# Kernel optimization log

Measured on AMD Instinct MI355X. Metric: run time of the kernel, lower is better.

Reference implementation:

```python
import jax, jax.numpy as jnp
import numpy as np

B, D, N, K = 16, 128, 4096, 1024


def setup_inputs() -> dict:
    key = jax.random.key(0)
    k1, k2 = jax.random.split(key)
    ze = jax.random.normal(k1, (B, D, N), dtype=jnp.float32)
    emb = jax.random.normal(k2, (K, D), dtype=jnp.float32)
    return {"ze": ze, "emb": emb}


def reference(ze, emb):
    """VQ forward: nearest-codebook quantization with straight-through estimator.

    ze:  (B, D, N) encoder latents (D = n_latent_dim, N = timesteps)
    emb: (K, D) codebook (stop-gradient applied, matching StopGrad on emb)
    returns zq_rg: (B, D, N) quantized latents; gradient flows straight to ze
    (ReplaceGrad: zq gets zero grad, ze gets the output grad).
    """
    emb_sg = jax.lax.stop_gradient(emb)
    # Squared L2 distance via expansion, avoiding the (B, D, K, N) broadcast:
    # d2[b,k,n] = ||ze[b,:,n]||^2 + ||emb[k]||^2 - 2 <ze[b,:,n], emb[k]>
    ze_sq = jnp.sum(ze * ze, axis=1)            # (B, N)
    emb_sq = jnp.sum(emb_sg * emb_sg, axis=1)   # (K,)
    dot = jnp.einsum('bdn,kd->bkn', ze, emb_sg)  # (B, K, N)
    d2 = ze_sq[:, None, :] + emb_sq[None, :, None] - 2.0 * dot
    ind = jnp.argmin(d2, axis=1)                # (B, N) nearest codebook index
    zq = jnp.transpose(jnp.take(emb_sg, ind, axis=0), (0, 2, 1))  # (B, D, N)
    # ReplaceGrad straight-through: value of zq, gradient routed to ze.
    zq_rg = ze + jax.lax.stop_gradient(zq - ze)
    return zq_rg
```

## Files before the change

kernel.cpp:

```cpp
#include <hip/hip_runtime.h>
#include <hip/hip_bf16.h>
#include <math.h>

#define BB 16
#define DD 128
#define NN 4096
#define KK 1024
#define CADD 320.0f
#define TAU 0.45f

typedef __attribute__((ext_vector_type(8))) short short8;
typedef __attribute__((ext_vector_type(4))) float f32x4;

static __device__ __forceinline__ unsigned short f32_bf16_rne(float f) {
    unsigned u = __float_as_uint(f);
    u += 0x7FFF + ((u >> 16) & 1);
    return (unsigned short)(u >> 16);
}
static __device__ __forceinline__ unsigned umin32(unsigned a, unsigned b) { return a < b ? a : b; }
static __device__ __forceinline__ unsigned umax32(unsigned a, unsigned b) { return a > b ? a : b; }
static __device__ __forceinline__ unsigned umed3(unsigned a, unsigned b, unsigned c) {
    unsigned d;
    asm("v_med3_u32 %0, %1, %2, %3" : "=v"(d) : "v"(a), "v"(b), "v"(c));
    return d;
}

__global__ void emb_sq_kernel(const float* __restrict__ emb,
                              float* __restrict__ e2) {
    int k = blockIdx.x * 256 + threadIdx.x;
    if (k >= KK) return;
    const float4* row = reinterpret_cast<const float4*>(emb + (size_t)k * DD);
    float a0 = 0.f, a1 = 0.f, a2 = 0.f, a3 = 0.f;
#pragma unroll
    for (int i = 0; i < DD / 16; ++i) {
        float4 v0 = row[i * 4 + 0];
        float4 v1 = row[i * 4 + 1];
        float4 v2 = row[i * 4 + 2];
        float4 v3 = row[i * 4 + 3];
        a0 += v0.x * v0.x + v0.y * v0.y + v0.z * v0.z + v0.w * v0.w;
        a1 += v1.x * v1.x + v1.y * v1.y + v1.z * v1.z + v1.w * v1.w;
        a2 += v2.x * v2.x + v2.y * v2.y + v2.z * v2.z + v2.w * v2.w;
        a3 += v3.x * v3.x + v3.y * v3.y + v3.z * v3.z + v3.w * v3.w;
    }
    e2[k] = (a0 + a1) + (a2 + a3) + CADD;
}

__global__ void emb_pack_kernel(const float* __restrict__ emb,
                                short* __restrict__ epk) {
    int g = blockIdx.x * 256 + threadIdx.x;
    int lane = g & 63;
    int s    = (g >> 6) & 3;
    int t    = g >> 8;
    int k = t * 16 + (lane & 15);
    int d = s * 32 + ((lane >> 4) & 3) * 8;
    const float* src = emb + (size_t)k * DD + d;
    short8 h;
#pragma unroll
    for (int j = 0; j < 8; ++j) h[j] = (short)f32_bf16_rne(-2.0f * src[j]);
    *reinterpret_cast<short8*>(epk + (size_t)g * 8) = h;
}

#define CEU(a, b) { unsigned lo_ = umin32(a, b), hi_ = umax32(a, b); (a) = lo_; (b) = hi_; }
#define MRG9(A1, A2, A3, A4, B1, B2, B3, B4) \
    CEU(A1, B1) CEU(A2, B2) CEU(A3, B3) CEU(A4, B4) \
    CEU(A3, B1) CEU(A4, B2) \
    CEU(A2, A3) \
    CEU(A4, B1) \
    CEU(A3, A4)

__global__ __launch_bounds__(256, 4)
void vq_mfma(const float* __restrict__ ze, const float* __restrict__ emb,
             const short* __restrict__ epk, const float* __restrict__ e2,
             float* __restrict__ out) {
    __shared__ __align__(16) char ubuf[(DD + 1) * 32 * 4];
    __shared__ unsigned kbuf[4][32][4];
    __shared__ int winner_s[32];
    __shared__ int rlist[32];
    __shared__ int rcnt;

    short* zstage = reinterpret_cast<short*>(ubuf);

    const int tid  = threadIdx.x;
    const int lane = tid & 63;
    const int wave = tid >> 6;
    const int b    = blockIdx.x >> 7;
    const int n0b  = (blockIdx.x & 127) * 32;
    const float* zb = ze + (size_t)b * DD * NN;

    const int nq = lane & 15;
    const int dq = (lane >> 4) & 3;

    float* e2w = reinterpret_cast<float*>(ubuf + 8192) + wave * 256;

#pragma unroll
    for (int cg = 0; cg < 2; ++cg) {
        const int col = n0b + cg * 16 + nq;
        const int d0  = wave * 32 + dq * 8;
        const float* zp = zb + (size_t)d0 * NN + col;
        short8 h;
#pragma unroll
        for (int j = 0; j < 8; ++j) h[j] = (short)f32_bf16_rne(zp[(size_t)j * NN]);
        *reinterpret_cast<short8*>(zstage + (cg * 256 + wave * 64 + lane) * 8) = h;
    }
#pragma unroll
    for (int i = 0; i < 4; ++i)
        e2w[i * 64 + lane] = e2[wave * 256 + i * 64 + lane];
    __syncthreads();

    short8 zf[2][4];
#pragma unroll
    for (int cg = 0; cg < 2; ++cg)
#pragma unroll
        for (int s = 0; s < 4; ++s)
            zf[cg][s] = *reinterpret_cast<const short8*>(
                zstage + ((cg * 4 + s) * 64 + lane) * 8);
    __syncthreads();

    unsigned K1[2], K2[2];
    K1[0] = K1[1] = K2[0] = K2[1] = 0xFFFFFFFFu;

    const int t0 = wave * 16;
    const short* ep = epk + (size_t)(t0 * 4) * 512 + (size_t)lane * 8;
    unsigned kb = (unsigned)(t0 * 16 + dq * 4);

    short8 Af[3][4];
#pragma unroll
    for (int s = 0; s < 4; ++s)
        Af[0][s] = *reinterpret_cast<const short8*>(ep + s * 512);
#pragma unroll
    for (int s = 0; s < 4; ++s)
        Af[1][s] = *reinterpret_cast<const short8*>(ep + 2048 + s * 512);

    float4 evC = *reinterpret_cast<const float4*>(e2w + dq * 4);

#pragma unroll
    for (int tt = 0; tt < 16; ++tt) {
        const int cur = tt % 3;
        if (tt < 14) {
            const int nxt = (tt + 2) % 3;
            const short* epn = ep + (size_t)(tt + 2) * 2048;
#pragma unroll
            for (int s = 0; s < 4; ++s)
                Af[nxt][s] = *reinterpret_cast<const short8*>(epn + s * 512);
            asm volatile("s_waitcnt vmcnt(8)" ::: "memory");
        } else if (tt == 14) {
            asm volatile("s_waitcnt vmcnt(4)" ::: "memory");
        } else {
            asm volatile("s_waitcnt vmcnt(0)" ::: "memory");
        }
        __builtin_amdgcn_sched_barrier(0);

        const float4 evN = (tt < 15)
            ? *reinterpret_cast<const float4*>(e2w + (tt + 1) * 16 + dq * 4)
            : evC;

        f32x4 acc0 = {evC.x, evC.y, evC.z, evC.w};
        f32x4 acc1 = acc0;
#define STEP(AF, S) \
        acc0 = __builtin_amdgcn_mfma_f32_16x16x32_bf16(AF, zf[0][S], acc0, 0, 0, 0); \
        acc1 = __builtin_amdgcn_mfma_f32_16x16x32_bf16(AF, zf[1][S], acc1, 0, 0, 0);
        STEP(Af[cur][0], 0) STEP(Af[cur][1], 1) STEP(Af[cur][2], 2) STEP(Af[cur][3], 3)
#undef STEP

#pragma unroll
        for (int cg = 0; cg < 2; ++cg) {
            const f32x4 a = (cg == 0) ? acc0 : acc1;
#pragma unroll
            for (int r = 0; r < 4; ++r) {
                const unsigned x = (__float_as_uint(a[r]) & 0xFFFFFC00u) | (kb + r);
                K2[cg] = umed3(K1[cg], K2[cg], x);
                K1[cg] = umin32(K1[cg], x);
            }
        }
        kb += 16;
        evC = evN;
    }

    unsigned T1[2], T2[2], T3[2], T4[2];
#pragma unroll
    for (int cg = 0; cg < 2; ++cg) {
        unsigned A1 = K1[cg], A2 = K2[cg];
        unsigned B1 = __shfl_xor(A1, 16);
        unsigned B2 = __shfl_xor(A2, 16);
        CEU(A1, B1) CEU(A2, B2) CEU(A2, B1)
        unsigned C1 = __shfl_xor(A1, 32);
        unsigned C2 = __shfl_xor(A2, 32);
        unsigned C3 = __shfl_xor(B1, 32);
        unsigned C4 = __shfl_xor(B2, 32);
        MRG9(A1, A2, B1, B2, C1, C2, C3, C4)
        T1[cg] = A1; T2[cg] = A2; T3[cg] = B1; T4[cg] = B2;
    }

    if (lane < 32) {
        const int cgid = lane >> 4;
        kbuf[wave][lane][0] = cgid ? T1[1] : T1[0];
        kbuf[wave][lane][1] = cgid ? T2[1] : T2[0];
        kbuf[wave][lane][2] = cgid ? T3[1] : T3[0];
        kbuf[wave][lane][3] = cgid ? T4[1] : T4[0];
    }
    __syncthreads();

    if (wave == 0) {
        const int c = lane & 31;
        unsigned A1 = kbuf[0][c][0], A2 = kbuf[0][c][1];
        unsigned A3 = kbuf[0][c][2], A4 = kbuf[0][c][3];
#pragma unroll
        for (int q = 1; q < 4; ++q) {
            unsigned B1 = kbuf[q][c][0], B2 = kbuf[q][c][1];
            unsigned B3 = kbuf[q][c][2], B4 = kbuf[q][c][3];
            MRG9(A1, A2, A3, A4, B1, B2, B3, B4)
        }
        const float M1 = __uint_as_float(A1 & 0xFFFFFC00u);
        const float M2 = __uint_as_float(A2 & 0xFFFFFC00u);
        const bool trig = (lane < 32) && ((M2 - M1) < TAU);
        if (lane < 32) {
            winner_s[c] = (int)(A1 & 0x3FFu);
            kbuf[0][c][0] = A1; kbuf[0][c][1] = A2;
            kbuf[0][c][2] = A3; kbuf[0][c][3] = A4;
        }
        const unsigned long long mask = __ballot(trig);
        if (trig) {
            const int idx = __popcll(mask & ((1ull << lane) - 1ull));
            rlist[idx] = c;
        }
        if (lane == 0) rcnt = (int)__popcll(mask);
    }
    __syncthreads();

    {
        const int rc = rcnt;
        for (int j = wave; j < rc; j += 4) {
            const int c = rlist[j];
            const int coln = n0b + c;
            const int I0 = (int)(kbuf[0][c][0] & 0x3FFu);
            const int I1 = (int)(kbuf[0][c][1] & 0x3FFu);
            const int I2 = (int)(kbuf[0][c][2] & 0x3FFu);
            const int I3 = (int)(kbuf[0][c][3] & 0x3FFu);
            double s0 = 0.0, s1 = 0.0, s2 = 0.0, s3 = 0.0;
#pragma unroll
            for (int h = 0; h < 2; ++h) {
                const int d = h * 64 + lane;
                const double zv = (double)zb[(size_t)d * NN + coln];
                double q;
                q = zv - (double)emb[(size_t)I0 * DD + d]; s0 += q * q;
                q = zv - (double)emb[(size_t)I1 * DD + d]; s1 += q * q;
                q = zv - (double)emb[(size_t)I2 * DD + d]; s2 += q * q;
                q = zv - (double)emb[(size_t)I3 * DD + d]; s3 += q * q;
            }
#pragma unroll
            for (int off = 1; off < 64; off <<= 1) {
                s0 += __shfl_xor(s0, off);
                s1 += __shfl_xor(s1, off);
                s2 += __shfl_xor(s2, off);
                s3 += __shfl_xor(s3, off);
            }
            int best = I0; double db = s0;
            if (s1 < db || (s1 == db && I1 < best)) { db = s1; best = I1; }
            if (s2 < db || (s2 == db && I2 < best)) { db = s2; best = I2; }
            if (s3 < db || (s3 == db && I3 < best)) { db = s3; best = I3; }
            if (lane == 0) winner_s[c] = best;
        }
    }
    __syncthreads();

    float (*ew)[DD + 1] = reinterpret_cast<float(*)[DD + 1]>(ubuf);
#pragma unroll 2
    for (int rr = 0; rr < 8; ++rr) {
        const int r = wave * 8 + rr;
        const int idx = winner_s[r];
        ew[r][lane]      = emb[(size_t)idx * DD + lane];
        ew[r][lane + 64] = emb[(size_t)idx * DD + lane + 64];
    }
    __syncthreads();

    {
        const int c = lane & 31;
        const int coln = n0b + c;
#pragma unroll 4
        for (int dd = 0; dd < 16; ++dd) {
            const int d = wave * 32 + dd * 2 + (lane >> 5);
            const float zv = zb[(size_t)d * NN + coln];
            const float evv = ew[c][d];
            out[((size_t)b * DD + d) * NN + coln] = zv + (evv - zv);
        }
    }
}

extern "C" void kernel_launch(void* const* d_in, const int* in_sizes, int n_in,
                              void* d_out, int out_size, void* d_ws, size_t ws_size,
                              hipStream_t stream) {
    (void)in_sizes; (void)n_in; (void)out_size; (void)ws_size;
    const float* ze  = (const float*)d_in[0];
    const float* emb = (const float*)d_in[1];
    float*       out = (float*)d_out;

    char* ws = (char*)d_ws;
    short* epk = (short*)ws;
    float* e2  = (float*)(ws + (size_t)KK * DD * 2);

    emb_sq_kernel<<<KK / 256, 256, 0, stream>>>(emb, e2);
    emb_pack_kernel<<<(KK * DD / 8) / 256, 256, 0, stream>>>(emb, epk);
    vq_mfma<<<(BB * NN) / 32, 256, 0, stream>>>(ze, emb, epk, e2, out);
}
```

Baseline: 47.37 us.

## Process all codebook entries in a single wave per block, removing cross-wave merges

Shrinks each block from four waves to one, so a single wave scans all 1024 codebook entries for its 32 columns. This removes the LDS staging of z, the cross-wave top-4 merge and every __syncthreads. The codebook prefetch drops from triple to double buffering, and the output gather now runs in two 64-dimension passes through a smaller LDS tile. In exchange, far fewer waves are resident per SIMD and each wave runs a loop four times longer, so there is less parallelism to hide MFMA and memory latency.

```diff
diff --git a/kernel.cpp b/kernel.cpp
--- a/kernel.cpp
+++ b/kernel.cpp
@@ -68,90 +68,68 @@
     CEU(A4, B1) \
     CEU(A3, A4)
 
-__global__ __launch_bounds__(256, 4)
+__global__ __launch_bounds__(64, 4)
 void vq_mfma(const float* __restrict__ ze, const float* __restrict__ emb,
              const short* __restrict__ epk, const float* __restrict__ e2,
              float* __restrict__ out) {
-    __shared__ __align__(16) char ubuf[(DD + 1) * 32 * 4];
-    __shared__ unsigned kbuf[4][32][4];
-    __shared__ int winner_s[32];
-    __shared__ int rlist[32];
-    __shared__ int rcnt;
-
-    short* zstage = reinterpret_cast<short*>(ubuf);
-
-    const int tid  = threadIdx.x;
-    const int lane = tid & 63;
-    const int wave = tid >> 6;
+    __shared__ __align__(16) char lds_[12544];
+    float (*ew)[65] = reinterpret_cast<float(*)[65]>(lds_);
+    float* e2l      = reinterpret_cast<float*>(lds_ + 8320);
+    int*   winner   = reinterpret_cast<int*>(lds_ + 12416);
+
+    const int lane = threadIdx.x;
     const int b    = blockIdx.x >> 7;
-    const int n0b  = (blockIdx.x & 127) * 32;
+    const int n0   = (blockIdx.x & 127) * 32;
     const float* zb = ze + (size_t)b * DD * NN;
 
     const int nq = lane & 15;
     const int dq = (lane >> 4) & 3;
 
-    float* e2w = reinterpret_cast<float*>(ubuf + 8192) + wave * 256;
-
+#pragma unroll
+    for (int i = 0; i < 4; ++i) {
+        float4 v = *reinterpret_cast<const float4*>(e2 + i * 256 + lane * 4);
+        *reinterpret_cast<float4*>(e2l + i * 256 + lane * 4) = v;
+    }
+
+    short8 zf[2][4];
 #pragma unroll
     for (int cg = 0; cg < 2; ++cg) {
-        const int col = n0b + cg * 16 + nq;
-        const int d0  = wave * 32 + dq * 8;
-        const float* zp = zb + (size_t)d0 * NN + col;
-        short8 h;
-#pragma unroll
-        for (int j = 0; j < 8; ++j) h[j] = (short)f32_bf16_rne(zp[(size_t)j * NN]);
-        *reinterpret_cast<short8*>(zstage + (cg * 256 + wave * 64 + lane) * 8) = h;
-    }
-#pragma unroll
-    for (int i = 0; i < 4; ++i)
-        e2w[i * 64 + lane] = e2[wave * 256 + i * 64 + lane];
-    __syncthreads();
-
-    short8 zf[2][4];
-#pragma unroll
-    for (int cg = 0; cg < 2; ++cg)
-#pragma unroll
-        for (int s = 0; s < 4; ++s)
-            zf[cg][s] = *reinterpret_cast<const short8*>(
-                zstage + ((cg * 4 + s) * 64 + lane) * 8);
-    __syncthreads();
+        const int col = n0 + cg * 16 + nq;
+#pragma unroll
+        for (int s = 0; s < 4; ++s) {
+            const float* zp = zb + (size_t)(s * 32 + dq * 8) * NN + col;
+#pragma unroll
+            for (int j = 0; j < 8; ++j)
+                zf[cg][s][j] = (short)f32_bf16_rne(zp[(size_t)j * NN]);
+        }
+    }
 
     unsigned K1[2], K2[2];
     K1[0] = K1[1] = K2[0] = K2[1] = 0xFFFFFFFFu;
 
-    const int t0 = wave * 16;
-    const short* ep = epk + (size_t)(t0 * 4) * 512 + (size_t)lane * 8;
-    unsigned kb = (unsigned)(t0 * 16 + dq * 4);
-
-    short8 Af[3][4];
-#pragma unroll
-    for (int s = 0; s < 4; ++s)
+    const short* ep = epk + (size_t)lane * 8;
+    unsigned kb = (unsigned)(dq * 4);
+
+    short8 Af[2][4];
+#pragma unroll
+    for (int s = 0; s < 4; ++s) {
         Af[0][s] = *reinterpret_cast<const short8*>(ep + s * 512);
-#pragma unroll
-    for (int s = 0; s < 4; ++s)
         Af[1][s] = *reinterpret_cast<const short8*>(ep + 2048 + s * 512);
-
-    float4 evC = *reinterpret_cast<const float4*>(e2w + dq * 4);
-
-#pragma unroll
-    for (int tt = 0; tt < 16; ++tt) {
-        const int cur = tt % 3;
-        if (tt < 14) {
-            const int nxt = (tt + 2) % 3;
-            const short* epn = ep + (size_t)(tt + 2) * 2048;
-#pragma unroll
-            for (int s = 0; s < 4; ++s)
-                Af[nxt][s] = *reinterpret_cast<const short8*>(epn + s * 512);
-            asm volatile("s_waitcnt vmcnt(8)" ::: "memory");
-        } else if (tt == 14) {
+    }
+    float4 evC = *reinterpret_cast<const float4*>(e2l + dq * 4);
+
+#pragma unroll 2
+    for (int tt = 0; tt < 64; ++tt) {
+        const int cur = tt & 1;
+        if (tt < 63) {
             asm volatile("s_waitcnt vmcnt(4)" ::: "memory");
         } else {
             asm volatile("s_waitcnt vmcnt(0)" ::: "memory");
         }
         __builtin_amdgcn_sched_barrier(0);
 
-        const float4 evN = (tt < 15)
-            ? *reinterpret_cast<const float4*>(e2w + (tt + 1) * 16 + dq * 4)
+        const float4 evN = (tt < 63)
+            ? *reinterpret_cast<const float4*>(e2l + (tt + 1) * 16 + dq * 4)
             : evC;
 
         f32x4 acc0 = {evC.x, evC.y, evC.z, evC.w};
@@ -161,6 +139,14 @@
         acc1 = __builtin_amdgcn_mfma_f32_16x16x32_bf16(AF, zf[1][S], acc1, 0, 0, 0);
         STEP(Af[cur][0], 0) STEP(Af[cur][1], 1) STEP(Af[cur][2], 2) STEP(Af[cur][3], 3)
 #undef STEP
+
+        {
+            const int tn = (tt < 62) ? (tt + 2) : 63;
+            const short* epn = ep + (size_t)tn * 2048;
+#pragma unroll
+            for (int s = 0; s < 4; ++s)
+                Af[cur][s] = *reinterpret_cast<const short8*>(epn + s * 512);
+        }
 
 #pragma unroll
         for (int cg = 0; cg < 2; ++cg) {
@@ -191,51 +177,27 @@
         T1[cg] = A1; T2[cg] = A2; T3[cg] = B1; T4[cg] = B2;
     }
 
-    if (lane < 32) {
-        const int cgid = lane >> 4;
-        kbuf[wave][lane][0] = cgid ? T1[1] : T1[0];
-        kbuf[wave][lane][1] = cgid ? T2[1] : T2[0];
-        kbuf[wave][lane][2] = cgid ? T3[1] : T3[0];
-        kbuf[wave][lane][3] = cgid ? T4[1] : T4[0];
-    }
-    __syncthreads();
-
-    if (wave == 0) {
+    const int cgid = (lane >> 4) & 1;
+    const unsigned S1 = cgid ? T1[1] : T1[0];
+    const unsigned S2 = cgid ? T2[1] : T2[0];
+    const unsigned S3 = cgid ? T3[1] : T3[0];
+    const unsigned S4 = cgid ? T4[1] : T4[0];
+    {
         const int c = lane & 31;
-        unsigned A1 = kbuf[0][c][0], A2 = kbuf[0][c][1];
-        unsigned A3 = kbuf[0][c][2], A4 = kbuf[0][c][3];
-#pragma unroll
-        for (int q = 1; q < 4; ++q) {
-            unsigned B1 = kbuf[q][c][0], B2 = kbuf[q][c][1];
-            unsigned B3 = kbuf[q][c][2], B4 = kbuf[q][c][3];
-            MRG9(A1, A2, A3, A4, B1, B2, B3, B4)
-        }
-        const float M1 = __uint_as_float(A1 & 0xFFFFFC00u);
-        const float M2 = __uint_as_float(A2 & 0xFFFFFC00u);
+        if (lane < 32) winner[c] = (int)(S1 & 0x3FFu);
+        const float M1 = __uint_as_float(S1 & 0xFFFFFC00u);
+        const float M2 = __uint_as_float(S2 & 0xFFFFFC00u);
         const bool trig = (lane < 32) && ((M2 - M1) < TAU);
-        if (lane < 32) {
-            winner_s[c] = (int)(A1 & 0x3FFu);
-            kbuf[0][c][0] = A1; kbuf[0][c][1] = A2;
-            kbuf[0][c][2] = A3; kbuf[0][c][3] = A4;
-        }
-        const unsigned long long mask = __ballot(trig);
-        if (trig) {
-            const int idx = __popcll(mask & ((1ull << lane) - 1ull));
-            rlist[idx] = c;
-        }
-        if (lane == 0) rcnt = (int)__popcll(mask);
-    }
-    __syncthreads();
-
-    {
-        const int rc = rcnt;
-        for (int j = wave; j < rc; j += 4) {
-            const int c = rlist[j];
-            const int coln = n0b + c;
-            const int I0 = (int)(kbuf[0][c][0] & 0x3FFu);
-            const int I1 = (int)(kbuf[0][c][1] & 0x3FFu);
-            const int I2 = (int)(kbuf[0][c][2] & 0x3FFu);
-            const int I3 = (int)(kbuf[0][c][3] & 0x3FFu);
+        unsigned m32 = (unsigned)(__ballot(trig) & 0xFFFFFFFFull);
+
+        while (m32) {
+            const int c2 = __builtin_ctz(m32);
+            m32 &= m32 - 1;
+            const int I0 = (int)((unsigned)__shfl((int)S1, c2) & 0x3FFu);
+            const int I1 = (int)((unsigned)__shfl((int)S2, c2) & 0x3FFu);
+            const int I2 = (int)((unsigned)__shfl((int)S3, c2) & 0x3FFu);
+            const int I3 = (int)((unsigned)__shfl((int)S4, c2) & 0x3FFu);
+            const int coln = n0 + c2;
             double s0 = 0.0, s1 = 0.0, s2 = 0.0, s3 = 0.0;
 #pragma unroll
             for (int h = 0; h < 2; ++h) {
@@ -258,30 +220,30 @@
             if (s1 < db || (s1 == db && I1 < best)) { db = s1; best = I1; }
             if (s2 < db || (s2 == db && I2 < best)) { db = s2; best = I2; }
             if (s3 < db || (s3 == db && I3 < best)) { db = s3; best = I3; }
-            if (lane == 0) winner_s[c] = best;
-        }
-    }
-    __syncthreads();
-
-    float (*ew)[DD + 1] = reinterpret_cast<float(*)[DD + 1]>(ubuf);
-#pragma unroll 2
-    for (int rr = 0; rr < 8; ++rr) {
-        const int r = wave * 8 + rr;
-        const int idx = winner_s[r];
-        ew[r][lane]      = emb[(size_t)idx * DD + lane];
-        ew[r][lane + 64] = emb[(size_t)idx * DD + lane + 64];
-    }
-    __syncthreads();
-
-    {
-        const int c = lane & 31;
-        const int coln = n0b + c;
+            if (lane == 0) winner[c2] = best;
+        }
+    }
+
+#pragma unroll 1
+    for (int pass = 0; pass < 2; ++pass) {
+        const int dbase = pass * 64;
 #pragma unroll 4
-        for (int dd = 0; dd < 16; ++dd) {
-            const int d = wave * 32 + dd * 2 + (lane >> 5);
-            const float zv = zb[(size_t)d * NN + coln];
-            const float evv = ew[c][d];
-            out[((size_t)b * DD + d) * NN + coln] = zv + (evv - zv);
+        for (int rr = 0; rr < 32; ++rr) {
+            const int idx = winner[rr];
+            ew[rr][lane] = emb[(size_t)idx * DD + dbase + lane];
+        }
+        {
+            const int c = lane & 31;
+            const int half = lane >> 5;
+            const int coln = n0 + c;
+#pragma unroll 4
+            for (int dd = 0; dd < 32; ++dd) {
+                const int dl = dd * 2 + half;
+                const int d  = dbase + dl;
+                const float zv  = zb[(size_t)d * NN + coln];
+                const float evv = ew[c][dl];
+                out[((size_t)b * DD + d) * NN + coln] = zv + (evv - zv);
+            }
         }
     }
 }
@@ -300,5 +262,5 @@
 
     emb_sq_kernel<<<KK / 256, 256, 0, stream>>>(emb, e2);
     emb_pack_kernel<<<(KK * DD / 8) / 256, 256, 0, stream>>>(emb, epk);
-    vq_mfma<<<(BB * NN) / 32, 256, 0, stream>>>(ze, emb, epk, e2, out);
-}
+    vq_mfma<<<(BB * NN) / 32, 64, 0, stream>>>(ze, emb, epk, e2, out);
+}
```

Result: slower. 67.59 us (+42.7%).
